# Kernel tuning notes

Measured on AMD Instinct MI355X. Metric: run time of the kernel, lower is better.

Reference implementation:

```python
import jax, jax.numpy as jnp
import numpy as np
from math import sqrt

B, IN_C, OUT_C, H, W, WDIM, K = 16, 512, 512, 64, 64, 512, 3
EPS = 1e-8
LRELU_SLOPE = 0.2


def setup_inputs() -> dict:
    key = jax.random.key(0)
    ks = jax.random.split(key, 5)
    return {
        "x": jax.random.normal(ks[0], (B, IN_C, H, W), dtype=jnp.float32),
        "w": jax.random.normal(ks[1], (B, WDIM), dtype=jnp.float32),
        "noise": jax.random.normal(ks[2], (B, 1, H, W), dtype=jnp.float32),
        "linear_w": jax.random.normal(ks[3], (IN_C, WDIM), dtype=jnp.float32),
        "linear_b": jnp.ones((IN_C,), dtype=jnp.float32),
        "conv_w": jax.random.normal(ks[4], (OUT_C, IN_C, K, K), dtype=jnp.float32),
        "scale_noise": jnp.zeros((OUT_C,), dtype=jnp.float32),
        "bias": jnp.zeros((OUT_C,), dtype=jnp.float32),
    }


def reference(x, w, noise, linear_w, linear_b, conv_w, scale_noise, bias):
    # EqualizerStraights: equalized-lr linear, scale = 1/sqrt(w_dim)
    s = w @ (linear_w * (1.0 / sqrt(WDIM))).T + linear_b  # [b, in_c]
    # Weight_Demod: equalized conv weight, scale = 1/sqrt(in_c*k*k)
    base_w = conv_w * (1.0 / sqrt(IN_C * K * K))  # [out, in, k, k]
    weights = base_w[None] * s[:, None, :, None, None]  # [b, out, in, k, k]
    sigma_inv = jax.lax.rsqrt(
        jnp.sum(weights * weights, axis=(2, 3, 4), keepdims=True) + EPS)
    weights = weights * sigma_inv

    def conv1(xi, wi):  # xi [in,h,w], wi [out,in,k,k]
        return jax.lax.conv_general_dilated(
            xi[None], wi, window_strides=(1, 1), padding="SAME",
            dimension_numbers=("NCHW", "OIHW", "NCHW"))[0]

    y = jax.vmap(conv1)(x, weights)  # [b, out, h, w]
    y = y + scale_noise[None, :, None, None] * noise
    return jax.nn.leaky_relu(y + bias[None, :, None, None], negative_slope=LRELU_SLOPE)
```

## Files before the change

### kernel.cpp

```cpp
#include <hip/hip_runtime.h>
#include <hip/hip_bf16.h>
#include <stdint.h>

typedef __bf16 bf16_t;
typedef __bf16 bf16x8 __attribute__((ext_vector_type(8)));
typedef short short8 __attribute__((ext_vector_type(8)));
typedef float f32x4 __attribute__((ext_vector_type(4)));

#define RS512  0.044194173824159216f
#define RS4608 0.014731391274719739f

__global__ void k_style(const float* __restrict__ w, const float* __restrict__ lw,
                        const float* __restrict__ lb, float* __restrict__ s) {
  int b = blockIdx.y;
  int c = blockIdx.x * 256 + threadIdx.x;
  const float4* wr = (const float4*)(w + b * 512);
  const float4* lr = (const float4*)(lw + (size_t)c * 512);
  float acc = 0.f;
#pragma unroll 4
  for (int d = 0; d < 128; ++d) {
    float4 a = wr[d], q = lr[d];
    acc += a.x * q.x + a.y * q.y + a.z * q.z + a.w * q.w;
  }
  s[b * 512 + c] = acc * RS512 + lb[c];
}

__global__ void k_wprep(const float* __restrict__ cw, float* __restrict__ wsq,
                        bf16_t* __restrict__ bwf, f32x4* __restrict__ zb) {
  if (blockIdx.x == 0) zb[threadIdx.x] = (f32x4)0.f;
  int idx = blockIdx.x * 256 + threadIdx.x;
  int o = idx >> 9, i = idx & 511;
  float v[9];
  float ss = 0.f;
#pragma unroll
  for (int t = 0; t < 9; ++t) {
    float x = cw[(size_t)idx * 9 + t] * RS4608;
    v[t] = x;
    ss += x * x;
  }
  wsq[idx] = ss;
  int lane = (o & 15) | (((i >> 3) & 3) << 4);
  int base_blk = (i >> 5) * 32 + (o >> 4);
#pragma unroll
  for (int t = 0; t < 9; ++t) {
    size_t e = ((size_t)(t * 512 + base_blk) << 9) + lane * 8 + (i & 7);
    bwf[e] = (bf16_t)v[t];
  }
}

__global__ void k_sigma(const float* __restrict__ s, const float* __restrict__ wsq,
                        float* __restrict__ sinv) {
  __shared__ float s2[512];
  int b = blockIdx.y;
  int o = blockIdx.x * 256 + threadIdx.x;
  for (int i = threadIdx.x; i < 512; i += 256) {
    float v = s[b * 512 + i];
    s2[i] = v * v;
  }
  __syncthreads();
  const float4* qr = (const float4*)(wsq + (size_t)o * 512);
  float acc = 0.f;
#pragma unroll 4
  for (int d = 0; d < 128; ++d) {
    float4 q = qr[d];
    acc += q.x * s2[4 * d] + q.y * s2[4 * d + 1] + q.z * s2[4 * d + 2] + q.w * s2[4 * d + 3];
  }
  sinv[b * 512 + o] = rsqrtf(acc + 1e-8f);
}

__global__ void k_xt(const float* __restrict__ x, const float* __restrict__ s,
                     bf16_t* __restrict__ xt) {
  int ic = blockIdx.x, h = blockIdx.y, b = blockIdx.z;
  __shared__ __align__(16) bf16_t tile[8192];
  int t = threadIdx.x;
  int wcol = t & 63;
  int g = t >> 6;
#pragma unroll
  for (int blk = 0; blk < 4; ++blk) {
    int grp = blk * 4 + g;
    bf16x8 vec;
#pragma unroll
    for (int k = 0; k < 8; ++k) {
      int i = ic * 128 + grp * 8 + k;
      float v = x[(((size_t)b * 512 + i) * 64 + h) * 64 + wcol] * s[b * 512 + i];
      vec[k] = (bf16_t)v;
    }
    *(bf16x8*)((char*)tile + grp * 1024 + wcol * 16) = vec;
  }
  __syncthreads();
  char* dst = (char*)xt + ((((size_t)b * 64 + h) * 16 + ic * 4) << 12) + g * 1024 + wcol * 16;
#pragma unroll
  for (int j = 0; j < 4; ++j) {
    bf16x8 v = *(bf16x8*)((char*)tile + (j * 4 + g) * 1024 + wcol * 16);
    *(bf16x8*)(dst + j * 4096) = v;
  }
}

#define AS1 __attribute__((address_space(1)))
#define AS3 __attribute__((address_space(3)))

__device__ __forceinline__ void gl16(const void* g, void* l) {
  __builtin_amdgcn_global_load_lds((const AS1 void*)g, (AS3 void*)l, 16, 0, 0);
}

#define VMCNT(n) asm volatile("s_waitcnt vmcnt(" #n ")" ::: "memory")

#define XT0 4096u

__global__ __launch_bounds__(512, 4) void k_conv(
    const char* __restrict__ wsb,
    const bf16_t* __restrict__ bwf,
    const float* __restrict__ sinv, const float* __restrict__ noise,
    const float* __restrict__ snz, const float* __restrict__ bias,
    float* __restrict__ out) {
  __shared__ __align__(16) char lds[51200];

  const int t = threadIdx.x;
  const int rq = blockIdx.x;
  const int OY = blockIdx.y;
  const int b = blockIdx.z;
  const int h0 = rq * 4;
  const int lane = t & 63;
  const int wv = t >> 6;
  const int wm = wv & 1;
  const int wn = wv >> 1;

  f32x4 acc[4][4] = {};
  bf16x8 wA[4], wB[4];

  uint32_t xsoff[3], xdst[3], xsel[3];
#pragma unroll
  for (int k = 0; k < 3; ++k) {
    int slot = wv * 3 + k, row = slot >> 2, q = slot & 3;
    int gr = h0 - 1 + row;
    int valid = ((unsigned)gr < 64u) ? 1 : 0;
    uint32_t so = valid ? (XT0 + (uint32_t)b * 4194304u + (uint32_t)gr * 65536u +
                           (uint32_t)q * 1024u)
                        : 0u;
    xsoff[k] = __builtin_amdgcn_readfirstlane(so);
    xdst[k] = __builtin_amdgcn_readfirstlane((uint32_t)(1024 + row * 4096 + q * 1024));
    xsel[k] = __builtin_amdgcn_readfirstlane((uint32_t)valid);
  }

  auto stX = [&](int k, uint32_t cxoff, int xb) {
    uint32_t co = xsel[k] ? cxoff : 0u;
    gl16(wsb + xsoff[k] + co + (size_t)(lane * 16), lds + xdst[k] + (uint32_t)(xb * 24576));
  };

  const size_t wbase0 = ((size_t)(OY * 8 + wm * 4)) << 10;
  auto loadW = [&](int tap, int c, bf16x8* d) {
    const char* p = (const char*)bwf + wbase0 + (((size_t)(tap * 16 + c)) << 15) +
                    (size_t)(lane * 16);
#pragma unroll
    for (int mi = 0; mi < 4; ++mi)
      d[mi] = *(const bf16x8*)(p + mi * 1024);
  };

  const uint32_t pXbase =
      (uint32_t)(1024 + wn * 4096 + (lane >> 4) * 1024 + (lane & 15) * 16);
  const bool c0 = (lane & 15) == 0;
  const bool c15 = (lane & 15) == 15;

#define CTAP(J, XB, AF)                                                        \
  {                                                                            \
    const int ky = (J) / 3, kx = (J) % 3;                                      \
    __builtin_amdgcn_s_setprio(1);                                             \
    _Pragma("unroll") for (int col = 0; col < 4; ++col) {                      \
      short8 xv = *(const short8*)(lds + pXbase +                              \
                                   (uint32_t)((XB) * 24576 + ky * 4096 +       \
                                              col * 256 + (kx - 1) * 16));     \
      if (kx == 0 && col == 0) xv = c0 ? (short8)0 : xv;                       \
      if (kx == 2 && col == 3) xv = c15 ? (short8)0 : xv;                      \
      bf16x8 bv = __builtin_bit_cast(bf16x8, xv);                              \
      _Pragma("unroll") for (int mi = 0; mi < 4; ++mi)                         \
          acc[mi][col] = __builtin_amdgcn_mfma_f32_16x16x32_bf16(              \
              AF[mi], bv, acc[mi][col], 0, 0, 0);                              \
    }                                                                          \
    __builtin_amdgcn_s_setprio(0);                                             \
  }

#define CHUNK(C, XB, P, LAST)                                                  \
  {                                                                            \
    _Pragma("unroll") for (int j = 0; j < 9; ++j) {                            \
      if (!(LAST) && j < 3) stX(j, (uint32_t)(((C) + 1) * 4096), (XB) ^ 1);    \
      if (j < 8) {                                                             \
        if (((j + (P)) & 1) == 0) loadW(j + 1, (C), wB);                       \
        else loadW(j + 1, (C), wA);                                            \
      } else if (!(LAST)) {                                                    \
        if (((j + (P)) & 1) == 0) loadW(0, (C) + 1, wB);                       \
        else loadW(0, (C) + 1, wA);                                            \
      }                                                                        \
      if (((j + (P)) & 1) == 0) CTAP(j, (XB), wA)                              \
      else CTAP(j, (XB), wB)                                                   \
    }                                                                          \
    if (!(LAST)) { VMCNT(4); __builtin_amdgcn_s_barrier(); }                   \
  }

#pragma unroll
  for (int k = 0; k < 3; ++k) stX(k, 0u, 0);
  loadW(0, 0, wA);
  VMCNT(4);
  __builtin_amdgcn_s_barrier();

#pragma unroll 1
  for (int ci = 0; ci < 7; ++ci) {
    const int c = ci * 2;
    CHUNK(c, 0, 0, 0);
    CHUNK(c + 1, 1, 1, 0);
  }
  CHUNK(14, 0, 0, 0);
  CHUNK(15, 1, 1, 1);

  const float* sb = sinv + b * 512;
  const int og = OY * 128 + wm * 64 + ((lane >> 4) << 2);
  const int colb = lane & 15;
  const int prow = h0 + wn;
  float nzv[4];
#pragma unroll
  for (int col = 0; col < 4; ++col)
    nzv[col] = noise[(size_t)b * 4096 + prow * 64 + col * 16 + colb];
#pragma unroll
  for (int mi = 0; mi < 4; ++mi) {
#pragma unroll
    for (int r = 0; r < 4; ++r) {
      int o = og + mi * 16 + r;
      float sv = sb[o];
      float nw = snz[o];
      float bv = bias[o];
      float* orow = out + (((size_t)b * 512 + o) * 64 + prow) * 64;
#pragma unroll
      for (int col = 0; col < 4; ++col) {
        float v = acc[mi][col][r] * sv + nw * nzv[col] + bv;
        orow[col * 16 + colb] = v > 0.f ? v : 0.2f * v;
      }
    }
  }
}

extern "C" void kernel_launch(void* const* d_in, const int* in_sizes, int n_in,
                              void* d_out, int out_size, void* d_ws, size_t ws_size,
                              hipStream_t stream) {
  const float* x     = (const float*)d_in[0];
  const float* w     = (const float*)d_in[1];
  const float* noise = (const float*)d_in[2];
  const float* lw    = (const float*)d_in[3];
  const float* lb    = (const float*)d_in[4];
  const float* cw    = (const float*)d_in[5];
  const float* snz   = (const float*)d_in[6];
  const float* bias  = (const float*)d_in[7];
  float* out = (float*)d_out;

  char* ws = (char*)d_ws;
  char*   zbuf = ws;
  bf16_t* xt   = (bf16_t*)(ws + 4096);
  bf16_t* bwf  = (bf16_t*)(ws + 67112960);
  float*  s    = (float*)(ws + 71831552);
  float*  sinv = (float*)(ws + 71864320);
  float*  wsq  = (float*)(ws + 71897088);

  k_style<<<dim3(2, 16), 256, 0, stream>>>(w, lw, lb, s);
  k_wprep<<<dim3(1024), 256, 0, stream>>>(cw, wsq, bwf, (f32x4*)zbuf);
  k_sigma<<<dim3(2, 16), 256, 0, stream>>>(s, wsq, sinv);
  k_xt<<<dim3(4, 64, 16), 256, 0, stream>>>(x, s, xt);
  k_conv<<<dim3(16, 4, 16), 512, 0, stream>>>(ws, bwf, sinv, noise, snz, bias, out);
}
```

Before: 311.8 us.

## Stage conv weights through LDS with triple-buffered async loads; vectorize xt transpose

The conv kernel no longer loads weight fragments from global memory straight into registers. Each wave now issues async global-to-LDS copies of one weight slice per tap into a 3-slab ring, with per-tap vmcnt waits and a barrier before every tap. This shares each weight load across the block and drops the wA/wB register double buffer, at the cost of more LDS (74752 B) and nine barriers per channel chunk. The x-transpose kernel now reads x with float4 loads, hoists the style scales, and XOR-swizzles the LDS tile to reduce bank conflicts.

```diff
diff --git a/kernel.cpp b/kernel.cpp
--- a/kernel.cpp
+++ b/kernel.cpp
@@ -73,25 +73,40 @@
   int ic = blockIdx.x, h = blockIdx.y, b = blockIdx.z;
   __shared__ __align__(16) bf16_t tile[8192];
   int t = threadIdx.x;
-  int wcol = t & 63;
-  int g = t >> 6;
-#pragma unroll
-  for (int blk = 0; blk < 4; ++blk) {
-    int grp = blk * 4 + g;
-    bf16x8 vec;
+  int q = t & 15;
+  int ig = t >> 4;
+
+  float sc[8];
+  const float* sp = s + b * 512 + ic * 128 + ig * 8;
+#pragma unroll
+  for (int k = 0; k < 8; ++k) sc[k] = sp[k];
+
+  float4 m[8];
+  const float* xp = x + (((size_t)(b * 512 + ic * 128 + ig * 8)) << 12) + h * 64 + q * 4;
+#pragma unroll
+  for (int k = 0; k < 8; ++k) m[k] = *(const float4*)(xp + (size_t)k * 4096);
+
+#pragma unroll
+  for (int j = 0; j < 4; ++j) {
+    bf16x8 v;
 #pragma unroll
     for (int k = 0; k < 8; ++k) {
-      int i = ic * 128 + grp * 8 + k;
-      float v = x[(((size_t)b * 512 + i) * 64 + h) * 64 + wcol] * s[b * 512 + i];
-      vec[k] = (bf16_t)v;
+      float e = (j == 0 ? m[k].x : j == 1 ? m[k].y : j == 2 ? m[k].z : m[k].w) * sc[k];
+      v[k] = (bf16_t)e;
     }
-    *(bf16x8*)((char*)tile + grp * 1024 + wcol * 16) = vec;
+    uint32_t a = (uint32_t)(ig * 1024 + (q * 4 + j) * 16);
+    a ^= ((a >> 6) & 7u) << 4;
+    *(bf16x8*)((char*)tile + a) = v;
   }
   __syncthreads();
+
+  int wcol = t & 63, g = t >> 6;
   char* dst = (char*)xt + ((((size_t)b * 64 + h) * 16 + ic * 4) << 12) + g * 1024 + wcol * 16;
 #pragma unroll
   for (int j = 0; j < 4; ++j) {
-    bf16x8 v = *(bf16x8*)((char*)tile + (j * 4 + g) * 1024 + wcol * 16);
+    uint32_t a = (uint32_t)((j * 4 + g) * 1024 + wcol * 16);
+    a ^= ((a >> 6) & 7u) << 4;
+    bf16x8 v = *(bf16x8*)((char*)tile + a);
     *(bf16x8*)(dst + j * 4096) = v;
   }
 }
@@ -104,16 +119,16 @@
 }
 
 #define VMCNT(n) asm volatile("s_waitcnt vmcnt(" #n ")" ::: "memory")
+#define BAR __builtin_amdgcn_s_barrier()
 
 #define XT0 4096u
 
 __global__ __launch_bounds__(512, 4) void k_conv(
-    const char* __restrict__ wsb,
-    const bf16_t* __restrict__ bwf,
+    const char* __restrict__ wsb, const bf16_t* __restrict__ bwf,
     const float* __restrict__ sinv, const float* __restrict__ noise,
     const float* __restrict__ snz, const float* __restrict__ bias,
     float* __restrict__ out) {
-  __shared__ __align__(16) char lds[51200];
+  __shared__ __align__(16) char lds[74752];
 
   const int t = threadIdx.x;
   const int rq = blockIdx.x;
@@ -126,7 +141,6 @@
   const int wn = wv >> 1;
 
   f32x4 acc[4][4] = {};
-  bf16x8 wA[4], wB[4];
 
   uint32_t xsoff[3], xdst[3], xsel[3];
 #pragma unroll
@@ -138,7 +152,7 @@
                            (uint32_t)q * 1024u)
                         : 0u;
     xsoff[k] = __builtin_amdgcn_readfirstlane(so);
-    xdst[k] = __builtin_amdgcn_readfirstlane((uint32_t)(1024 + row * 4096 + q * 1024));
+    xdst[k] = __builtin_amdgcn_readfirstlane((uint32_t)(24576 + row * 4096 + q * 1024));
     xsel[k] = __builtin_amdgcn_readfirstlane((uint32_t)valid);
   }
 
@@ -147,23 +161,24 @@
     gl16(wsb + xsoff[k] + co + (size_t)(lane * 16), lds + xdst[k] + (uint32_t)(xb * 24576));
   };
 
-  const size_t wbase0 = ((size_t)(OY * 8 + wm * 4)) << 10;
-  auto loadW = [&](int tap, int c, bf16x8* d) {
-    const char* p = (const char*)bwf + wbase0 + (((size_t)(tap * 16 + c)) << 15) +
-                    (size_t)(lane * 16);
-#pragma unroll
-    for (int mi = 0; mi < 4; ++mi)
-      d[mi] = *(const bf16x8*)(p + mi * 1024);
+  const char* wgsrc = (const char*)bwf + ((OY * 8 + wv) << 10) + (lane << 4);
+  auto stW = [&](uint32_t srcoff, int slab) {
+    gl16(wgsrc + srcoff, lds + slab * 8192 + (wv << 10));
   };
 
+  const uint32_t woff = (uint32_t)((wm << 12) + (lane << 4));
   const uint32_t pXbase =
-      (uint32_t)(1024 + wn * 4096 + (lane >> 4) * 1024 + (lane & 15) * 16);
+      (uint32_t)(24576 + wn * 4096 + (lane >> 4) * 1024 + (lane & 15) * 16);
   const bool c0 = (lane & 15) == 0;
   const bool c15 = (lane & 15) == 15;
 
-#define CTAP(J, XB, AF)                                                        \
+#define CTAP(J, XB)                                                            \
   {                                                                            \
     const int ky = (J) / 3, kx = (J) % 3;                                      \
+    bf16x8 af[4];                                                              \
+    _Pragma("unroll") for (int mi = 0; mi < 4; ++mi)                           \
+        af[mi] = *(const bf16x8*)(lds + (uint32_t)(((J) % 3) * 8192) + woff +  \
+                                  (uint32_t)(mi * 1024));                      \
     __builtin_amdgcn_s_setprio(1);                                             \
     _Pragma("unroll") for (int col = 0; col < 4; ++col) {                      \
       short8 xv = *(const short8*)(lds + pXbase +                              \
@@ -174,42 +189,51 @@
       bf16x8 bv = __builtin_bit_cast(bf16x8, xv);                              \
       _Pragma("unroll") for (int mi = 0; mi < 4; ++mi)                         \
           acc[mi][col] = __builtin_amdgcn_mfma_f32_16x16x32_bf16(              \
-              AF[mi], bv, acc[mi][col], 0, 0, 0);                              \
+              af[mi], bv, acc[mi][col], 0, 0, 0);                              \
     }                                                                          \
     __builtin_amdgcn_s_setprio(0);                                             \
   }
 
-#define CHUNK(C, XB, P, LAST)                                                  \
+#define PHASE(CWB, CXB, JC, LAST, XB)                                          \
   {                                                                            \
-    _Pragma("unroll") for (int j = 0; j < 9; ++j) {                            \
-      if (!(LAST) && j < 3) stX(j, (uint32_t)(((C) + 1) * 4096), (XB) ^ 1);    \
-      if (j < 8) {                                                             \
-        if (((j + (P)) & 1) == 0) loadW(j + 1, (C), wB);                       \
-        else loadW(j + 1, (C), wA);                                            \
-      } else if (!(LAST)) {                                                    \
-        if (((j + (P)) & 1) == 0) loadW(0, (C) + 1, wB);                       \
-        else loadW(0, (C) + 1, wA);                                            \
-      }                                                                        \
-      if (((j + (P)) & 1) == 0) CTAP(j, (XB), wA)                              \
-      else CTAP(j, (XB), wB)                                                   \
+    if ((JC) + 2 <= 8) stW((CWB) + (uint32_t)((JC) + 2) * 524288u, ((JC) + 2) % 3); \
+    else if (!(LAST)) stW((CWB) + 32768u + (uint32_t)((JC) - 7) * 524288u, ((JC) + 2) % 3); \
+    if (!(LAST) && (JC) < 3) stX((JC), (CXB), (XB) ^ 1);                       \
+    if (LAST) {                                                                \
+      if ((JC) <= 6) { VMCNT(2); }                                             \
+      else if ((JC) == 7) { VMCNT(1); }                                        \
+      else { VMCNT(0); }                                                       \
+    } else {                                                                   \
+      if ((JC) == 0 || (JC) == 4) { VMCNT(3); }                                \
+      else if ((JC) == 1 || (JC) == 3) { VMCNT(4); }                           \
+      else if ((JC) == 2) { VMCNT(5); }                                        \
+      else { VMCNT(2); }                                                       \
     }                                                                          \
-    if (!(LAST)) { VMCNT(4); __builtin_amdgcn_s_barrier(); }                   \
+    __builtin_amdgcn_s_barrier();                                              \
+    CTAP((JC), (XB));                                                          \
   }
 
 #pragma unroll
   for (int k = 0; k < 3; ++k) stX(k, 0u, 0);
-  loadW(0, 0, wA);
-  VMCNT(4);
-  __builtin_amdgcn_s_barrier();
-
+  stW(0u, 0);
+  stW(524288u, 1);
+  VMCNT(0); BAR;
+
+  uint32_t cwb = 0, cxb = 4096;
 #pragma unroll 1
   for (int ci = 0; ci < 7; ++ci) {
-    const int c = ci * 2;
-    CHUNK(c, 0, 0, 0);
-    CHUNK(c + 1, 1, 1, 0);
-  }
-  CHUNK(14, 0, 0, 0);
-  CHUNK(15, 1, 1, 1);
+#pragma unroll
+    for (int jc = 0; jc < 9; ++jc) PHASE(cwb, cxb, jc, 0, 0);
+    cwb += 32768u; cxb += 4096u;
+#pragma unroll
+    for (int jc = 0; jc < 9; ++jc) PHASE(cwb, cxb, jc, 0, 1);
+    cwb += 32768u; cxb += 4096u;
+  }
+#pragma unroll
+  for (int jc = 0; jc < 9; ++jc) PHASE(cwb, cxb, jc, 0, 0);
+  cwb += 32768u;
+#pragma unroll
+  for (int jc = 0; jc < 9; ++jc) PHASE(cwb, 0u, jc, 1, 1);
 
   const float* sb = sinv + b * 512;
   const int og = OY * 128 + wm * 64 + ((lane >> 4) << 2);
```

Result: faster. 295.2 us (-5.3%).
